# Kernel tuning notes

Measured on AMD Instinct MI355X. Metric: run time of the kernel, lower is better.

Reference implementation:

```python
import jax, jax.numpy as jnp
import numpy as np

DIM, HEADS, HD = 256, 8, 32
WS, GT, SR = 8, 1, 2
B_, H0, W0 = 4, 128, 128
SCALE = HD ** -0.5


def _bilinear_up_align(x, s):
    # x: (B, C, h, w) -> (B, C, h*s, w*s), bilinear, align_corners=True (matches torch)
    B, C, h, w = x.shape
    oh, ow = h * s, w * s
    def coords(n, o):
        pos = jnp.arange(o, dtype=jnp.float32) * ((n - 1) / (o - 1))
        i0 = jnp.clip(jnp.floor(pos).astype(jnp.int32), 0, n - 2)
        t = pos - i0.astype(jnp.float32)
        return i0, t
    y0, ty = coords(h, oh)
    x0, tx = coords(w, ow)
    top = x[:, :, y0, :] * (1 - ty)[:, None] + x[:, :, y0 + 1, :] * ty[:, None]
    return top[:, :, :, x0] * (1 - tx) + top[:, :, :, x0 + 1] * tx


def _layernorm(x, w, b, eps=1e-5):
    mu = x.mean(-1, keepdims=True)
    var = x.var(-1, keepdims=True)
    return (x - mu) * jax.lax.rsqrt(var + eps) * w + b


def setup_inputs() -> dict:
    key = jax.random.key(0)
    ks = jax.random.split(key, 8)
    w = lambda k, shape: jax.random.normal(k, shape, jnp.float32) * 0.02
    return {
        "x": jax.random.normal(ks[0], (B_, H0 * W0, DIM), jnp.float32),
        "gt": jax.random.normal(ks[1], (B_, H0 // WS, W0 // WS, GT, DIM), jnp.float32),
        "q_w": w(ks[2], (DIM, DIM)), "q_b": jnp.zeros((DIM,), jnp.float32),
        "kv_w": w(ks[3], (2 * DIM, DIM)), "kv_b": jnp.zeros((2 * DIM,), jnp.float32),
        "sr_w": w(ks[4], (DIM, DIM, SR, SR)), "sr_b": jnp.zeros((DIM,), jnp.float32),
        "norm_w": jnp.ones((DIM,), jnp.float32), "norm_b": jnp.zeros((DIM,), jnp.float32),
        "proj_w": w(ks[5], (DIM, DIM)), "proj_b": jnp.zeros((DIM,), jnp.float32),
        "H": H0, "W": W0,
    }


def reference(x, gt, q_w, q_b, kv_w, kv_b, sr_w, sr_b, norm_w, norm_b, proj_w, proj_b, H, W):
    Bb, Np, C = x.shape
    nH, nW = H // WS, W // WS  # H, W multiples of WS -> no padding branch
    xm = x.reshape(Bb, H, W, C)
    # window partition -> (B, WS*WS, C), B = Bb*nH*nW
    xw = xm.reshape(Bb, nH, WS, nW, WS, C).transpose(0, 1, 3, 2, 4, 5).reshape(-1, WS * WS, C)
    g = gt.reshape(-1, GT, C)  # gt grid already matches (nH, nW)
    skip = g
    xc = jnp.concatenate([g, xw], axis=1)  # (B, N, C), N = GT + WS*WS
    B, N, _ = xc.shape
    q = (xc @ q_w.T + q_b).reshape(B, N, HEADS, HD).transpose(0, 2, 1, 3)  # (B,h,N,d)
    # spatial-reduction KV branch (sr_ratio > 1, gt_num != 0)
    x_ = xw.transpose(0, 2, 1).reshape(B, C, WS, WS)
    x_ = _bilinear_up_align(x_, SR)  # (B, C, WS*SR, WS*SR)
    x_ = jax.lax.conv_general_dilated(
        x_, sr_w, (SR, SR), "VALID",
        dimension_numbers=("NCHW", "OIHW", "NCHW")) + sr_b[None, :, None, None]  # (B,C,WS,WS)
    x_ = _layernorm(x_.reshape(B, C, -1).transpose(0, 2, 1), norm_w, norm_b)
    x_ = jnp.concatenate([g, x_], axis=1)  # (B, N, C)
    kv = (x_ @ kv_w.T + kv_b).reshape(B, -1, 2, HEADS, HD).transpose(2, 0, 3, 1, 4)
    k, v = kv[0], kv[1]  # (B,h,N,d)
    attn = jax.nn.softmax(jnp.einsum("bhnd,bhmd->bhnm", q, k) * SCALE, axis=-1)
    out = jnp.einsum("bhnm,bhmd->bhnd", attn, v).transpose(0, 2, 1, 3).reshape(B, N, C)
    out = out @ proj_w.T + proj_b
    gt_out = out[:, :GT, :]
    xo = out[:, GT:, :].reshape(Bb, nH, nW, WS, WS, C)
    xo = xo.transpose(0, 1, 3, 2, 4, 5).reshape(Bb, H, W, C)  # window reverse
    return xo.reshape(Bb, H * W, C), gt_out, skip
```

## Files before the change

### kernel.cpp

```cpp
#include <hip/hip_runtime.h>

typedef __attribute__((ext_vector_type(4))) float f32x4;
typedef __attribute__((ext_vector_type(8))) short bf16x8;
typedef __attribute__((ext_vector_type(2))) uint u32x2;

#define SCALE_ 0.17677669529663687f

__device__ __forceinline__ float bf2f(ushort u){
  union { unsigned i; float f; } v; v.i = ((unsigned)u) << 16; return v.f;
}
__device__ __forceinline__ ushort f2bf(float f){
  union { float f; unsigned i; } v; v.f = f;
  unsigned r = v.i + 0x7fffu + ((v.i >> 16) & 1u);
  return (ushort)(r >> 16);
}
__device__ __forceinline__ void gl16(const void* g, const ushort* l) {
  __builtin_amdgcn_global_load_lds((const __attribute__((address_space(1))) uint*)g,
                                   (__attribute__((address_space(3))) uint*)l, 16, 0, 0);
}

__global__ __launch_bounds__(256) void k_prep(const float* __restrict__ x,
    const float* __restrict__ gt, ushort* __restrict__ xc,
    ushort* __restrict__ xkv, float* __restrict__ out2)
{
  int row = blockIdx.x;
  int c = threadIdx.x;
  int wi = row / 65, n = row - wi * 65;
  if (n == 0) {
    float g = gt[(size_t)wi * 256 + c];
    ushort gb = f2bf(g);
    xc[(size_t)row * 256 + c] = gb;
    xkv[(size_t)row * 256 + c] = gb;
    out2[(size_t)wi * 256 + c] = g;
  } else {
    int s = n - 1, r = s >> 3, cc = s & 7;
    int b = wi >> 8, wh = (wi >> 4) & 15, ww = wi & 15;
    int hw = (wh * 8 + r) * 128 + ww * 8 + cc;
    xc[(size_t)row * 256 + c] = f2bf(x[((size_t)b * 16384 + hw) * 256 + c]);
  }
}

__global__ __launch_bounds__(256) void k_wprep(const float* __restrict__ qw,
    const float* __restrict__ kvw, const float* __restrict__ pw,
    const float* __restrict__ srw, ushort* __restrict__ wq,
    ushort* __restrict__ wkv, ushort* __restrict__ wpr, ushort* __restrict__ wcv)
{
  int i = blockIdx.x * 256 + threadIdx.x;
  if (i < 65536)            wq[i] = f2bf(qw[i]);
  else if (i < 196608)      wkv[i - 65536] = f2bf(kvw[i - 65536]);
  else if (i < 262144)      wpr[i - 196608] = f2bf(pw[i - 196608]);
  else {
    int j = i - 262144;
    int o = j >> 10, t = (j >> 8) & 3, cc = j & 255;
    wcv[j] = f2bf(srw[o * 1024 + cc * 4 + t]);
  }
}

template<int N>
__global__ __launch_bounds__(256) void k_gemm2(const ushort* __restrict__ A,
    const ushort* __restrict__ W, const float* __restrict__ bias,
    ushort* __restrict__ C)
{
  constexpr int K = 256;
  __shared__ __align__(16) ushort As[2][128 * 64];
  __shared__ __align__(16) ushort Bs[2][128 * 64];
  int lin = blockIdx.y * gridDim.x + blockIdx.x;
  int qq = (gridDim.x * gridDim.y) >> 3;
  int sw2 = (lin & 7) * qq + (lin >> 3);
  int m0 = (sw2 / gridDim.x) * 128, n0 = (sw2 % gridDim.x) * 128;
  int tid = threadIdx.x, lane = tid & 63;
  int wave = tid >> 6;
  int lm = lane & 15, kg = lane >> 4;
  int wr = wave >> 1, wc = wave & 1;

  const char* Ab = (const char*)A + (size_t)m0 * (K * 2);
  const char* Bb = (const char*)W + (size_t)n0 * (K * 2);

  auto stage = [&](int buf, int kt) {
#pragma unroll
    for (int j = 0; j < 4; ++j) {
      int c = j * 256 + tid;
      int row = c >> 3, slot = c & 7;
      int srcoff = row * (K * 2) + kt * 128 + ((slot * 16) ^ ((row & 7) << 4));
      gl16(Ab + srcoff, (const ushort*)((const char*)As[buf] + c * 16));
      gl16(Bb + srcoff, (const ushort*)((const char*)Bs[buf] + c * 16));
    }
  };

  f32x4 acc[4][4];
  f32x4 zero = {0.f, 0.f, 0.f, 0.f};
#pragma unroll
  for (int a = 0; a < 4; ++a)
#pragma unroll
    for (int b = 0; b < 4; ++b) acc[a][b] = zero;

  stage(0, 0);
  __syncthreads();
#pragma unroll
  for (int t = 0; t < 4; ++t) {
    int cur = t & 1;
    if (t < 3) stage(cur ^ 1, t + 1);
#pragma unroll
    for (int s = 0; s < 2; ++s) {
      int sw = (lm & 7) << 4;
      bf16x8 af[4], bw[4];
#pragma unroll
      for (int mi = 0; mi < 4; ++mi) {
        int row = wr * 64 + mi * 16 + lm;
        af[mi] = *(const bf16x8*)((const char*)As[cur] + row * 128 + ((s * 64 + kg * 16) ^ sw));
      }
#pragma unroll
      for (int ni = 0; ni < 4; ++ni) {
        int row = wc * 64 + ni * 16 + lm;
        bw[ni] = *(const bf16x8*)((const char*)Bs[cur] + row * 128 + ((s * 64 + kg * 16) ^ sw));
      }
#pragma unroll
      for (int mi = 0; mi < 4; ++mi)
#pragma unroll
        for (int ni = 0; ni < 4; ++ni)
          acc[mi][ni] = __builtin_amdgcn_mfma_f32_16x16x32_bf16(af[mi], bw[ni], acc[mi][ni], 0, 0, 0);
    }
    __syncthreads();
  }

  int rbase = m0 + wr * 64 + kg * 4;
#pragma unroll
  for (int ni = 0; ni < 4; ++ni) {
    int col = n0 + wc * 64 + ni * 16 + lm;
    float bv = bias[col];
#pragma unroll
    for (int mi = 0; mi < 4; ++mi) {
#pragma unroll
      for (int r = 0; r < 4; ++r)
        C[(size_t)(rbase + mi * 16 + r) * N + col] = f2bf(acc[mi][ni][r] + bv);
    }
  }
}

__global__ __launch_bounds__(512) void k_conv(const ushort* __restrict__ xc,
    const ushort* __restrict__ wconv, ushort* __restrict__ cconv)
{
  __shared__ ushort U[2][64 * 256];
  int wi = blockIdx.x;
  int tid = threadIdx.x, wave = tid >> 6, lane = tid & 63;
  int lm = lane & 15, kg = lane >> 4;
  const ushort* src = xc + (size_t)(wi * 65 + 1) * 256;
  f32x4 acc[4][2];
  f32x4 zero = {0.f, 0.f, 0.f, 0.f};
#pragma unroll
  for (int a = 0; a < 4; a++)
#pragma unroll
    for (int b = 0; b < 2; b++) acc[a][b] = zero;

  int cb = (tid & 31) * 8;
  int sg = tid >> 5;

  auto build = [&](int t, ushort* Ub) {
    int dy = t >> 1, dx = t & 1;
    for (int s = sg; s < 64; s += 16) {
      int i = s >> 3, j = s & 7;
      int yy = 2 * i + dy, xx = 2 * j + dx;
      float py = yy * (7.0f / 15.0f); int iy = (int)py; if (iy > 6) iy = 6; float ty = py - iy;
      float px = xx * (7.0f / 15.0f); int ix = (int)px; if (ix > 6) ix = 6; float tx = px - ix;
      float w00 = (1.f - ty) * (1.f - tx), w01 = (1.f - ty) * tx;
      float w10 = ty * (1.f - tx), w11 = ty * tx;
      const ushort* p = src + (size_t)(iy * 8 + ix) * 256 + cb;
      bf16x8 p00 = *(const bf16x8*)(p);
      bf16x8 p01 = *(const bf16x8*)(p + 256);
      bf16x8 p10 = *(const bf16x8*)(p + 2048);
      bf16x8 p11 = *(const bf16x8*)(p + 2304);
      bf16x8 o8;
#pragma unroll
      for (int jj = 0; jj < 8; jj++) {
        float v = w00 * bf2f((ushort)p00[jj]) + w01 * bf2f((ushort)p01[jj])
                + w10 * bf2f((ushort)p10[jj]) + w11 * bf2f((ushort)p11[jj]);
        o8[jj] = (short)f2bf(v);
      }
      int byteoff = s * 512 + ((2 * cb) ^ ((s & 7) << 4));
      *(bf16x8*)((char*)Ub + byteoff) = o8;
    }
  };

  build(0, U[0]);
  __syncthreads();
  for (int t = 0; t < 4; t++) {
    const ushort* Ub = U[t & 1];
    const ushort* wc = wconv + t * 256;
    for (int kk = 0; kk < 256; kk += 32) {
      int kb = kk + kg * 8;
      bf16x8 afr[4];
#pragma unroll
      for (int mi = 0; mi < 4; mi++) {
        int srow = mi * 16 + lm;
        int off = (srow * 512 + 2 * kb) ^ ((srow & 7) << 4);
        afr[mi] = *(const bf16x8*)((const char*)Ub + off);
      }
#pragma unroll
      for (int ni = 0; ni < 2; ni++) {
        bf16x8 b = *(const bf16x8*)(wc + (size_t)(wave * 32 + ni * 16 + lm) * 1024 + kb);
#pragma unroll
        for (int mi = 0; mi < 4; mi++)
          acc[mi][ni] = __builtin_amdgcn_mfma_f32_16x16x32_bf16(afr[mi], b, acc[mi][ni], 0, 0, 0);
      }
    }
    if (t < 3) build(t + 1, U[(t + 1) & 1]);
    __syncthreads();
  }

#pragma unroll
  for (int mi = 0; mi < 4; mi++) {
    int row = wi * 64 + mi * 16 + kg * 4;
#pragma unroll
    for (int ni = 0; ni < 2; ni++) {
      int col = wave * 32 + ni * 16 + lm;
#pragma unroll
      for (int r = 0; r < 4; r++)
        cconv[(size_t)(row + r) * 256 + col] = f2bf(acc[mi][ni][r]);
    }
  }
}

__global__ __launch_bounds__(256) void k_ln(const ushort* __restrict__ cconv,
    const float* __restrict__ srb, const float* __restrict__ nw,
    const float* __restrict__ nb, ushort* __restrict__ xkv)
{
  int row = blockIdx.x * 4 + (threadIdx.x >> 6);
  int lane = threadIdx.x & 63;
  const ushort* p = cconv + (size_t)row * 256;
  float v[4]; float sum = 0.f, sq = 0.f;
#pragma unroll
  for (int r = 0; r < 4; r++) {
    int c = r * 64 + lane;
    v[r] = bf2f(p[c]) + srb[c];
    sum += v[r]; sq += v[r] * v[r];
  }
#pragma unroll
  for (int off = 1; off < 64; off <<= 1) {
    sum += __shfl_xor(sum, off, 64);
    sq  += __shfl_xor(sq,  off, 64);
  }
  float mean = sum * (1.f / 256.f);
  float var = sq * (1.f / 256.f) - mean * mean;
  float rs = rsqrtf(var + 1e-5f);
  int wi = row >> 6, s = row & 63;
  ushort* o = xkv + (size_t)(wi * 65 + 1 + s) * 256;
#pragma unroll
  for (int r = 0; r < 4; r++) {
    int c = r * 64 + lane;
    o[c] = f2bf((v[r] - mean) * rs * nw[c] + nb[c]);
  }
}

__global__ __launch_bounds__(256) void k_attn(const ushort* __restrict__ q,
    const ushort* __restrict__ kv, ushort* __restrict__ att)
{
  __shared__ ushort smem[4][8064];
  int wi = blockIdx.x >> 1;
  int tid = threadIdx.x, wave = tid >> 6, lane = tid & 63;
  int h = (blockIdx.x & 1) * 4 + wave;
  int lm = lane & 15, kg = lane >> 4;
  ushort* plds = smem[wave];
  ushort* vt   = smem[wave] + 5760;

  size_t qbase  = (size_t)wi * 65 * 256 + (size_t)h * 32;
  size_t kvbase = (size_t)wi * 65 * 512 + (size_t)h * 32;

  for (int e = lane; e < 2080; e += 64) {
    int m = e >> 5, d = e & 31;
    vt[d * 72 + m] = kv[kvbase + (size_t)m * 512 + 256 + d];
  }

  bf16x8 akf[5], bqf[5];
#pragma unroll
  for (int i = 0; i < 5; i++) {
    akf[i] = *(const bf16x8*)(kv + kvbase + (size_t)(16 * i + lm) * 512 + kg * 8);
    bqf[i] = *(const bf16x8*)(q  + qbase  + (size_t)(16 * i + lm) * 256 + kg * 8);
  }

  f32x4 sc[5][5];
  f32x4 zero = {0.f, 0.f, 0.f, 0.f};
#pragma unroll
  for (int mi = 0; mi < 5; mi++)
#pragma unroll
    for (int nj = 0; nj < 5; nj++) sc[mi][nj] = zero;
#pragma unroll
  for (int mi = 0; mi < 5; mi++)
#pragma unroll
    for (int nj = 0; nj < 5; nj++)
      sc[mi][nj] = __builtin_amdgcn_mfma_f32_16x16x32_bf16(akf[mi], bqf[nj], sc[mi][nj], 0, 0, 0);

  const float C = SCALE_ * 1.4426950408889634f;
  float inv[5], p64b[5];
#pragma unroll
  for (int nj = 0; nj < 5; nj++) {
    float s4 = sc[4][nj][0];
    float mx = (kg == 0) ? s4 : -1e30f;
#pragma unroll
    for (int mi = 0; mi < 4; mi++)
#pragma unroll
      for (int r = 0; r < 4; r++) mx = fmaxf(mx, sc[mi][nj][r]);
    mx = fmaxf(mx, __shfl_xor(mx, 16, 64));
    mx = fmaxf(mx, __shfl_xor(mx, 32, 64));
    float sum = 0.f;
#pragma unroll
    for (int mi = 0; mi < 4; mi++)
#pragma unroll
      for (int r = 0; r < 4; r++) {
        float e = exp2f((sc[mi][nj][r] - mx) * C);
        sc[mi][nj][r] = e; sum += e;
      }
    float e4 = exp2f((s4 - mx) * C);
    sum += (kg == 0) ? e4 : 0.f;
    sum += __shfl_xor(sum, 16, 64);
    sum += __shfl_xor(sum, 32, 64);
    inv[nj] = 1.0f / sum;
    p64b[nj] = __shfl(e4, lm, 64);
  }

#pragma unroll
  for (int nj = 0; nj < 5; nj++) {
    int n = 16 * nj + lm;
#pragma unroll
    for (int mi = 0; mi < 4; mi++) {
      uint lo = (uint)f2bf(sc[mi][nj][0]) | ((uint)f2bf(sc[mi][nj][1]) << 16);
      uint hi = (uint)f2bf(sc[mi][nj][2]) | ((uint)f2bf(sc[mi][nj][3]) << 16);
      u32x2 pk = {lo, hi};
      *(u32x2*)(plds + n * 72 + 16 * mi + 4 * kg) = pk;
    }
  }

  f32x4 od[2][5];
#pragma unroll
  for (int dt = 0; dt < 2; dt++)
#pragma unroll
    for (int nj = 0; nj < 5; nj++) od[dt][nj] = zero;
#pragma unroll
  for (int c = 0; c < 2; c++) {
    bf16x8 av[2], bp[5];
#pragma unroll
    for (int dt = 0; dt < 2; dt++)
      av[dt] = *(const bf16x8*)(vt + (16 * dt + lm) * 72 + c * 32 + kg * 8);
#pragma unroll
    for (int nj = 0; nj < 5; nj++)
      bp[nj] = *(const bf16x8*)(plds + (16 * nj + lm) * 72 + c * 32 + kg * 8);
#pragma unroll
    for (int dt = 0; dt < 2; dt++)
#pragma unroll
      for (int nj = 0; nj < 5; nj++)
        od[dt][nj] = __builtin_amdgcn_mfma_f32_16x16x32_bf16(av[dt], bp[nj], od[dt][nj], 0, 0, 0);
  }
  float v64[8];
#pragma unroll
  for (int dt = 0; dt < 2; dt++)
#pragma unroll
    for (int r = 0; r < 4; r++)
      v64[dt * 4 + r] = bf2f(vt[(16 * dt + 4 * kg + r) * 72 + 64]);
#pragma unroll
  for (int dt = 0; dt < 2; dt++)
#pragma unroll
    for (int nj = 0; nj < 5; nj++)
#pragma unroll
      for (int r = 0; r < 4; r++)
        od[dt][nj][r] += v64[dt * 4 + r] * p64b[nj];

#pragma unroll
  for (int nj = 0; nj < 5; nj++) {
    int n = 16 * nj + lm;
    float scl = inv[nj];
#pragma unroll
    for (int dt = 0; dt < 2; dt++) {
      uint lo = (uint)f2bf(od[dt][nj][0] * scl) | ((uint)f2bf(od[dt][nj][1] * scl) << 16);
      uint hi = (uint)f2bf(od[dt][nj][2] * scl) | ((uint)f2bf(od[dt][nj][3] * scl) << 16);
      u32x2 pk = {lo, hi};
      *(u32x2*)(plds + n * 40 + 16 * dt + 4 * kg) = pk;
    }
  }
  size_t abase = (size_t)wi * 65 * 256 + (size_t)h * 32;
  for (int e = lane; e < 1040; e += 64) {
    int n = e >> 4, d2 = e & 15;
    *(uint*)(att + abase + (size_t)n * 256 + 2 * d2) = *(const uint*)(plds + n * 40 + 2 * d2);
  }
}

__global__ __launch_bounds__(256) void k_scatter(const ushort* __restrict__ po,
    float* __restrict__ out)
{
  size_t e = (size_t)blockIdx.x * 256 + threadIdx.x;
  if (e < 16777216) {
    int c = (int)(e & 255);
    int hw = (int)((e >> 8) & 16383);
    int b = (int)(e >> 22);
    int hh = hw >> 7, wp = hw & 127;
    int wh = hh >> 3, r = hh & 7, ww = wp >> 3, cc = wp & 7;
    int wi = b * 256 + wh * 16 + ww;
    int n = 1 + r * 8 + cc;
    out[e] = bf2f(po[(size_t)(wi * 65 + n) * 256 + c]);
  } else {
    size_t e2 = e - 16777216;
    int wi = (int)(e2 >> 8), c = (int)(e2 & 255);
    out[e] = bf2f(po[(size_t)(wi * 65) * 256 + c]);
  }
}

extern "C" void kernel_launch(void* const* d_in, const int* in_sizes, int n_in,
                              void* d_out, int out_size, void* d_ws, size_t ws_size,
                              hipStream_t stream)
{
  const float* x    = (const float*)d_in[0];
  const float* gt   = (const float*)d_in[1];
  const float* q_w  = (const float*)d_in[2];
  const float* q_b  = (const float*)d_in[3];
  const float* kv_w = (const float*)d_in[4];
  const float* kv_b = (const float*)d_in[5];
  const float* sr_w = (const float*)d_in[6];
  const float* sr_b = (const float*)d_in[7];
  const float* nw   = (const float*)d_in[8];
  const float* nb   = (const float*)d_in[9];
  const float* p_w  = (const float*)d_in[10];
  const float* p_b  = (const float*)d_in[11];
  (void)in_sizes; (void)n_in; (void)out_size;

  if (ws_size < 204996608u) return;
  char* ws = (char*)d_ws;
  ushort* xc  = (ushort*)(ws);
  ushort* qb  = (ushort*)(ws + 34078720);
  ushort* xkv = (ushort*)(ws + 68157440);
  ushort* kv  = (ushort*)(ws + 102236160);
  ushort* ccv = (ushort*)(ws + 170393600);
  ushort* wq  = (ushort*)(ws + 203948032);
  ushort* wkv = (ushort*)(ws + 204079104);
  ushort* wpr = (ushort*)(ws + 204341248);
  ushort* wcv = (ushort*)(ws + 204472320);

  float* out = (float*)d_out;
  float* out2 = out + 16777216 + 262144;

  k_prep<<<66560, 256, 0, stream>>>(x, gt, xc, xkv, out2);
  k_wprep<<<2048, 256, 0, stream>>>(q_w, kv_w, p_w, sr_w, wq, wkv, wpr, wcv);
  k_gemm2<256><<<dim3(2, 520), 256, 0, stream>>>(xc, wq, q_b, qb);
  k_conv<<<1024, 512, 0, stream>>>(xc, wcv, ccv);
  k_ln<<<16384, 256, 0, stream>>>(ccv, sr_b, nw, nb, xkv);
  k_gemm2<512><<<dim3(4, 520), 256, 0, stream>>>(xkv, wkv, kv_b, kv);
  k_attn<<<2048, 256, 0, stream>>>(qb, kv, xc);
  k_gemm2<256><<<dim3(2, 520), 256, 0, stream>>>(xc, wpr, p_b, qb);
  k_scatter<<<66560, 256, 0, stream>>>(qb, out);
}
```

Before: 280.0 us.

## Separable bilinear upsample in conv kernel, build two taps per pass

The conv kernel's LDS builder now does the bilinear upsample separably. Each thread interpolates vertically once over a row strip of five source pixels, then produces eight horizontal outputs from those values. This cuts redundant global loads and multiplies compared with four-corner gathers per output. Each build now fills both dx phases for a given dy into the two LDS buffers, so the loop becomes two build/MFMA phases with an extra barrier and no build overlapped with MFMA. A launch-bounds occupancy hint of 4 is added, which may constrain registers given the larger per-thread H array.

```diff
diff --git a/kernel.cpp b/kernel.cpp
--- a/kernel.cpp
+++ b/kernel.cpp
@@ -137,14 +137,15 @@
   }
 }
 
-__global__ __launch_bounds__(512) void k_conv(const ushort* __restrict__ xc,
+__global__ __launch_bounds__(512, 4) void k_conv(const ushort* __restrict__ xc,
     const ushort* __restrict__ wconv, ushort* __restrict__ cconv)
 {
-  __shared__ ushort U[2][64 * 256];
+  __shared__ __align__(16) ushort U[2][64 * 256];
   int wi = blockIdx.x;
   int tid = threadIdx.x, wave = tid >> 6, lane = tid & 63;
   int lm = lane & 15, kg = lane >> 4;
   const ushort* src = xc + (size_t)(wi * 65 + 1) * 256;
+
   f32x4 acc[4][2];
   f32x4 zero = {0.f, 0.f, 0.f, 0.f};
 #pragma unroll
@@ -152,60 +153,77 @@
 #pragma unroll
     for (int b = 0; b < 2; b++) acc[a][b] = zero;
 
-  int cb = (tid & 31) * 8;
-  int sg = tid >> 5;
-
-  auto build = [&](int t, ushort* Ub) {
-    int dy = t >> 1, dx = t & 1;
-    for (int s = sg; s < 64; s += 16) {
-      int i = s >> 3, j = s & 7;
-      int yy = 2 * i + dy, xx = 2 * j + dx;
-      float py = yy * (7.0f / 15.0f); int iy = (int)py; if (iy > 6) iy = 6; float ty = py - iy;
+  int cg = lane & 31;
+  int half = lane >> 5;
+  int xh = wave & 1;
+  int yy2 = (wave >> 1) * 2 + half;
+
+  auto build = [&](int p) {
+    int yy = yy2 * 2 + p;
+    float py = yy * (7.0f / 15.0f); int iy = (int)py; if (iy > 6) iy = 6; float ty = py - iy;
+    int j0 = xh * 3;
+    const ushort* r0 = src + (size_t)(iy * 8 + j0) * 256 + cg * 8;
+    const ushort* r1 = r0 + 2048;
+    float H[5][8];
+#pragma unroll
+    for (int jj = 0; jj < 5; ++jj) {
+      bf16x8 a = *(const bf16x8*)(r0 + jj * 256);
+      bf16x8 b = *(const bf16x8*)(r1 + jj * 256);
+#pragma unroll
+      for (int e = 0; e < 8; ++e) {
+        float av = bf2f((ushort)a[e]);
+        H[jj][e] = av + ty * (bf2f((ushort)b[e]) - av);
+      }
+    }
+#pragma unroll
+    for (int xi = 0; xi < 8; ++xi) {
+      int xx = xh * 8 + xi;
       float px = xx * (7.0f / 15.0f); int ix = (int)px; if (ix > 6) ix = 6; float tx = px - ix;
-      float w00 = (1.f - ty) * (1.f - tx), w01 = (1.f - ty) * tx;
-      float w10 = ty * (1.f - tx), w11 = ty * tx;
-      const ushort* p = src + (size_t)(iy * 8 + ix) * 256 + cb;
-      bf16x8 p00 = *(const bf16x8*)(p);
-      bf16x8 p01 = *(const bf16x8*)(p + 256);
-      bf16x8 p10 = *(const bf16x8*)(p + 2048);
-      bf16x8 p11 = *(const bf16x8*)(p + 2304);
+      int hl = ix - j0;
       bf16x8 o8;
 #pragma unroll
-      for (int jj = 0; jj < 8; jj++) {
-        float v = w00 * bf2f((ushort)p00[jj]) + w01 * bf2f((ushort)p01[jj])
-                + w10 * bf2f((ushort)p10[jj]) + w11 * bf2f((ushort)p11[jj]);
-        o8[jj] = (short)f2bf(v);
-      }
-      int byteoff = s * 512 + ((2 * cb) ^ ((s & 7) << 4));
-      *(bf16x8*)((char*)Ub + byteoff) = o8;
+      for (int e = 0; e < 8; ++e) {
+        float lv = H[hl][e];
+        o8[e] = (short)f2bf(lv + tx * (H[hl + 1][e] - lv));
+      }
+      int s = yy2 * 8 + (xx >> 1);
+      int off = (xx & 1) * 32768 + s * 512 + ((cg * 16) ^ ((s & 7) << 4));
+      *(bf16x8*)((char*)U + off) = o8;
     }
   };
 
-  build(0, U[0]);
+  auto mfma_pair = [&](int p) {
+#pragma unroll
+    for (int tt = 0; tt < 2; ++tt) {
+      const ushort* Ub = U[tt];
+      const ushort* wc = wconv + (p * 2 + tt) * 256;
+      for (int kk = 0; kk < 256; kk += 32) {
+        int kb = kk + kg * 8;
+        bf16x8 afr[4];
+#pragma unroll
+        for (int mi = 0; mi < 4; mi++) {
+          int srow = mi * 16 + lm;
+          int off = (srow * 512 + 2 * kb) ^ ((srow & 7) << 4);
+          afr[mi] = *(const bf16x8*)((const char*)Ub + off);
+        }
+#pragma unroll
+        for (int ni = 0; ni < 2; ni++) {
+          bf16x8 b = *(const bf16x8*)(wc + (size_t)(wave * 32 + ni * 16 + lm) * 1024 + kb);
+#pragma unroll
+          for (int mi = 0; mi < 4; mi++)
+            acc[mi][ni] = __builtin_amdgcn_mfma_f32_16x16x32_bf16(afr[mi], b, acc[mi][ni], 0, 0, 0);
+        }
+      }
+    }
+  };
+
+  build(0);
   __syncthreads();
-  for (int t = 0; t < 4; t++) {
-    const ushort* Ub = U[t & 1];
-    const ushort* wc = wconv + t * 256;
-    for (int kk = 0; kk < 256; kk += 32) {
-      int kb = kk + kg * 8;
-      bf16x8 afr[4];
-#pragma unroll
-      for (int mi = 0; mi < 4; mi++) {
-        int srow = mi * 16 + lm;
-        int off = (srow * 512 + 2 * kb) ^ ((srow & 7) << 4);
-        afr[mi] = *(const bf16x8*)((const char*)Ub + off);
-      }
-#pragma unroll
-      for (int ni = 0; ni < 2; ni++) {
-        bf16x8 b = *(const bf16x8*)(wc + (size_t)(wave * 32 + ni * 16 + lm) * 1024 + kb);
-#pragma unroll
-        for (int mi = 0; mi < 4; mi++)
-          acc[mi][ni] = __builtin_amdgcn_mfma_f32_16x16x32_bf16(afr[mi], b, acc[mi][ni], 0, 0, 0);
-      }
-    }
-    if (t < 3) build(t + 1, U[(t + 1) & 1]);
-    __syncthreads();
-  }
+  mfma_pair(0);
+  __syncthreads();
+  build(1);
+  __syncthreads();
+  mfma_pair(1);
 
 #pragma unroll
   for (int mi = 0; mi < 4; mi++) {
```

Result: slower. 345.2 us (+23.3%).

## Stage conv source window in LDS and use separable bilinear interpolation

Applied to the files above, without the earlier changes.

The conv kernel now copies the 64x256 bf16 window into LDS with async global_load_lds, then builds each upsampled tap from LDS. It does the bilinear interpolation separably, with a vertical lerp per row that is reused across columns and horizontal weights fixed at compile time, instead of four global gathers per output. The double-buffered U tile becomes a single buffer, so build and MFMA no longer overlap and extra barriers are added. It also forces waves_per_eu(4,4).

```diff
diff --git a/kernel.cpp b/kernel.cpp
--- a/kernel.cpp
+++ b/kernel.cpp
@@ -1,6 +1,7 @@
 #include <hip/hip_runtime.h>
 
 typedef __attribute__((ext_vector_type(4))) float f32x4;
+typedef __attribute__((ext_vector_type(8))) float f32x8;
 typedef __attribute__((ext_vector_type(8))) short bf16x8;
 typedef __attribute__((ext_vector_type(2))) uint u32x2;
 
@@ -137,14 +138,89 @@
   }
 }
 
-__global__ __launch_bounds__(512) void k_conv(const ushort* __restrict__ xc,
+__device__ __forceinline__ f32x8 row_lerp(const char* srcS, int row, int cg, float ty) {
+  int a0 = row * 512 + ((cg * 16) ^ ((row & 7) << 4));
+  int a1 = (row + 8) * 512 + ((cg * 16) ^ ((row & 7) << 4));
+  bf16x8 a = *(const bf16x8*)(srcS + a0);
+  bf16x8 b = *(const bf16x8*)(srcS + a1);
+  f32x8 h;
+#pragma unroll
+  for (int e = 0; e < 8; ++e) {
+    float av = bf2f((ushort)a[e]);
+    h[e] = av + ty * (bf2f((ushort)b[e]) - av);
+  }
+  return h;
+}
+__device__ __forceinline__ void emit_u(char* U, const f32x8& Ha, const f32x8& Hb,
+                                       float tx, int s, int cg) {
+  bf16x8 o8;
+#pragma unroll
+  for (int e = 0; e < 8; ++e) {
+    float lv = Ha[e];
+    o8[e] = (short)f2bf(lv + tx * (Hb[e] - lv));
+  }
+  *(bf16x8*)(U + s * 512 + ((cg * 16) ^ ((s & 7) << 4))) = o8;
+}
+
+template<int XH, int DX>
+__device__ __forceinline__ void conv_build(const char* srcS, char* U,
+                                           int dy, int i, int cg)
+{
+  int yy = 2 * i + dy;
+  float py = yy * (7.0f / 15.0f);
+  int iy = (int)py; if (iy > 6) iy = 6;
+  float ty = py - iy;
+  constexpr int j0 = XH * 3;
+  int rb = iy * 8 + j0;
+  f32x8 H0 = row_lerp(srcS, rb + 0, cg, ty);
+  f32x8 H1 = row_lerp(srcS, rb + 1, cg, ty);
+  f32x8 H2 = row_lerp(srcS, rb + 2, cg, ty);
+  f32x8 H3 = row_lerp(srcS, rb + 3, cg, ty);
+  f32x8 H4 = row_lerp(srcS, rb + 4, cg, ty);
+  int sb = i * 8 + XH * 4;
+  if (XH == 0 && DX == 0) {
+    emit_u(U, H0, H1, 0.0f,        sb + 0, cg);
+    emit_u(U, H0, H1, 14.f / 15.f, sb + 1, cg);
+    emit_u(U, H1, H2, 13.f / 15.f, sb + 2, cg);
+    emit_u(U, H2, H3, 12.f / 15.f, sb + 3, cg);
+  } else if (XH == 0 && DX == 1) {
+    emit_u(U, H0, H1,  7.f / 15.f, sb + 0, cg);
+    emit_u(U, H1, H2,  6.f / 15.f, sb + 1, cg);
+    emit_u(U, H2, H3,  5.f / 15.f, sb + 2, cg);
+    emit_u(U, H3, H4,  4.f / 15.f, sb + 3, cg);
+  } else if (XH == 1 && DX == 0) {
+    emit_u(U, H0, H1, 11.f / 15.f, sb + 0, cg);
+    emit_u(U, H1, H2, 10.f / 15.f, sb + 1, cg);
+    emit_u(U, H2, H3,  9.f / 15.f, sb + 2, cg);
+    emit_u(U, H3, H4,  8.f / 15.f, sb + 3, cg);
+  } else {
+    emit_u(U, H1, H2,  3.f / 15.f, sb + 0, cg);
+    emit_u(U, H2, H3,  2.f / 15.f, sb + 1, cg);
+    emit_u(U, H3, H4,  1.f / 15.f, sb + 2, cg);
+    emit_u(U, H3, H4,  1.0f,       sb + 3, cg);
+  }
+}
+
+__global__ __launch_bounds__(512)
+__attribute__((amdgpu_waves_per_eu(4, 4)))
+void k_conv(const ushort* __restrict__ xc,
     const ushort* __restrict__ wconv, ushort* __restrict__ cconv)
 {
-  __shared__ ushort U[2][64 * 256];
+  __shared__ __align__(16) ushort srcS[64 * 256];
+  __shared__ __align__(16) ushort Ubuf[64 * 256];
   int wi = blockIdx.x;
   int tid = threadIdx.x, wave = tid >> 6, lane = tid & 63;
   int lm = lane & 15, kg = lane >> 4;
-  const ushort* src = xc + (size_t)(wi * 65 + 1) * 256;
+
+  const char* src_g = (const char*)(xc + (size_t)(wi * 65 + 1) * 256);
+#pragma unroll
+  for (int j = 0; j < 4; ++j) {
+    int c = j * 512 + tid;
+    int row = c >> 5, slot = c & 31;
+    int srcoff = row * 512 + ((slot * 16) ^ ((row & 7) << 4));
+    gl16(src_g + srcoff, (const ushort*)((const char*)srcS + c * 16));
+  }
+
   f32x4 acc[4][2];
   f32x4 zero = {0.f, 0.f, 0.f, 0.f};
 #pragma unroll
@@ -152,39 +228,11 @@
 #pragma unroll
     for (int b = 0; b < 2; b++) acc[a][b] = zero;
 
-  int cb = (tid & 31) * 8;
-  int sg = tid >> 5;
-
-  auto build = [&](int t, ushort* Ub) {
-    int dy = t >> 1, dx = t & 1;
-    for (int s = sg; s < 64; s += 16) {
-      int i = s >> 3, j = s & 7;
-      int yy = 2 * i + dy, xx = 2 * j + dx;
-      float py = yy * (7.0f / 15.0f); int iy = (int)py; if (iy > 6) iy = 6; float ty = py - iy;
-      float px = xx * (7.0f / 15.0f); int ix = (int)px; if (ix > 6) ix = 6; float tx = px - ix;
-      float w00 = (1.f - ty) * (1.f - tx), w01 = (1.f - ty) * tx;
-      float w10 = ty * (1.f - tx), w11 = ty * tx;
-      const ushort* p = src + (size_t)(iy * 8 + ix) * 256 + cb;
-      bf16x8 p00 = *(const bf16x8*)(p);
-      bf16x8 p01 = *(const bf16x8*)(p + 256);
-      bf16x8 p10 = *(const bf16x8*)(p + 2048);
-      bf16x8 p11 = *(const bf16x8*)(p + 2304);
-      bf16x8 o8;
-#pragma unroll
-      for (int jj = 0; jj < 8; jj++) {
-        float v = w00 * bf2f((ushort)p00[jj]) + w01 * bf2f((ushort)p01[jj])
-                + w10 * bf2f((ushort)p10[jj]) + w11 * bf2f((ushort)p11[jj]);
-        o8[jj] = (short)f2bf(v);
-      }
-      int byteoff = s * 512 + ((2 * cb) ^ ((s & 7) << 4));
-      *(bf16x8*)((char*)Ub + byteoff) = o8;
-    }
-  };
-
-  build(0, U[0]);
-  __syncthreads();
-  for (int t = 0; t < 4; t++) {
-    const ushort* Ub = U[t & 1];
+  int cg = tid & 31;
+  int i = (tid >> 5) & 7;
+  int xh = tid >> 8;
+
+  auto mfma_tap = [&](int t) {
     const ushort* wc = wconv + t * 256;
     for (int kk = 0; kk < 256; kk += 32) {
       int kb = kk + kg * 8;
@@ -193,7 +241,7 @@
       for (int mi = 0; mi < 4; mi++) {
         int srow = mi * 16 + lm;
         int off = (srow * 512 + 2 * kb) ^ ((srow & 7) << 4);
-        afr[mi] = *(const bf16x8*)((const char*)Ub + off);
+        afr[mi] = *(const bf16x8*)((const char*)Ubuf + off);
       }
 #pragma unroll
       for (int ni = 0; ni < 2; ni++) {
@@ -203,9 +251,29 @@
           acc[mi][ni] = __builtin_amdgcn_mfma_f32_16x16x32_bf16(afr[mi], b, acc[mi][ni], 0, 0, 0);
       }
     }
-    if (t < 3) build(t + 1, U[(t + 1) & 1]);
-    __syncthreads();
-  }
+  };
+
+  __syncthreads();
+
+  if (xh == 0) conv_build<0, 0>((const char*)srcS, (char*)Ubuf, 0, i, cg);
+  else         conv_build<1, 0>((const char*)srcS, (char*)Ubuf, 0, i, cg);
+  __syncthreads();
+  mfma_tap(0);
+  __syncthreads();
+  if (xh == 0) conv_build<0, 1>((const char*)srcS, (char*)Ubuf, 0, i, cg);
+  else         conv_build<1, 1>((const char*)srcS, (char*)Ubuf, 0, i, cg);
+  __syncthreads();
+  mfma_tap(1);
+  __syncthreads();
+  if (xh == 0) conv_build<0, 0>((const char*)srcS, (char*)Ubuf, 1, i, cg);
+  else         conv_build<1, 0>((const char*)srcS, (char*)Ubuf, 1, i, cg);
+  __syncthreads();
+  mfma_tap(2);
+  __syncthreads();
+  if (xh == 0) conv_build<0, 1>((const char*)srcS, (char*)Ubuf, 1, i, cg);
+  else         conv_build<1, 1>((const char*)srcS, (char*)Ubuf, 1, i, cg);
+  __syncthreads();
+  mfma_tap(3);
 
 #pragma unroll
   for (int mi = 0; mi < 4; mi++) {
```

Result: faster. 274.0 us (-2.2%).

## Fuse output projection with window-reverse scatter and merge weight prep into input prep

Applied to the files above, without the earlier changes.

The final projection GEMM now writes fp32 results straight to their window-reversed positions in the output, removing the bf16 intermediate and the separate scatter kernel. Weight conversion is folded into the input-prep kernel as extra blocks, and input prep is vectorised to float4 reads with four rows per block. This cuts one full read/write pass over a large activation tensor and two launches. The fused epilogue's stores are strided per row, so they may coalesce less well than the old scatter.

```diff
diff --git a/kernel.cpp b/kernel.cpp
--- a/kernel.cpp
+++ b/kernel.cpp
@@ -1,6 +1,7 @@
 #include <hip/hip_runtime.h>
 
 typedef __attribute__((ext_vector_type(4))) float f32x4;
+typedef __attribute__((ext_vector_type(8))) float f32x8;
 typedef __attribute__((ext_vector_type(8))) short bf16x8;
 typedef __attribute__((ext_vector_type(2))) uint u32x2;
 
@@ -20,39 +21,47 @@
 }
 
 __global__ __launch_bounds__(256) void k_prep(const float* __restrict__ x,
-    const float* __restrict__ gt, ushort* __restrict__ xc,
-    ushort* __restrict__ xkv, float* __restrict__ out2)
-{
-  int row = blockIdx.x;
-  int c = threadIdx.x;
+    const float* __restrict__ gt, const float* __restrict__ qw,
+    const float* __restrict__ kvw, const float* __restrict__ pw,
+    const float* __restrict__ srw, ushort* __restrict__ xc,
+    ushort* __restrict__ xkv, float* __restrict__ out2,
+    ushort* __restrict__ wq, ushort* __restrict__ wkv,
+    ushort* __restrict__ wpr, ushort* __restrict__ wcv)
+{
+  int blk = blockIdx.x;
+  int tid = threadIdx.x;
+  if (blk >= 16640) {
+    int i = (blk - 16640) * 256 + tid;
+    if (i < 65536)            wq[i] = f2bf(qw[i]);
+    else if (i < 196608)      wkv[i - 65536] = f2bf(kvw[i - 65536]);
+    else if (i < 262144)      wpr[i - 196608] = f2bf(pw[i - 196608]);
+    else {
+      int j = i - 262144;
+      int o = j >> 10, t = (j >> 8) & 3, cc = j & 255;
+      wcv[j] = f2bf(srw[o * 1024 + cc * 4 + t]);
+    }
+    return;
+  }
+  int row = blk * 4 + (tid >> 6);
+  int c4 = (tid & 63) * 4;
   int wi = row / 65, n = row - wi * 65;
   if (n == 0) {
-    float g = gt[(size_t)wi * 256 + c];
-    ushort gb = f2bf(g);
-    xc[(size_t)row * 256 + c] = gb;
-    xkv[(size_t)row * 256 + c] = gb;
-    out2[(size_t)wi * 256 + c] = g;
+    float4 g4 = *(const float4*)(gt + (size_t)wi * 256 + c4);
+    uint lo = (uint)f2bf(g4.x) | ((uint)f2bf(g4.y) << 16);
+    uint hi = (uint)f2bf(g4.z) | ((uint)f2bf(g4.w) << 16);
+    u32x2 pk = {lo, hi};
+    *(u32x2*)(xc  + (size_t)row * 256 + c4) = pk;
+    *(u32x2*)(xkv + (size_t)row * 256 + c4) = pk;
+    *(float4*)(out2 + (size_t)wi * 256 + c4) = g4;
   } else {
     int s = n - 1, r = s >> 3, cc = s & 7;
     int b = wi >> 8, wh = (wi >> 4) & 15, ww = wi & 15;
     int hw = (wh * 8 + r) * 128 + ww * 8 + cc;
-    xc[(size_t)row * 256 + c] = f2bf(x[((size_t)b * 16384 + hw) * 256 + c]);
-  }
-}
-
-__global__ __launch_bounds__(256) void k_wprep(const float* __restrict__ qw,
-    const float* __restrict__ kvw, const float* __restrict__ pw,
-    const float* __restrict__ srw, ushort* __restrict__ wq,
-    ushort* __restrict__ wkv, ushort* __restrict__ wpr, ushort* __restrict__ wcv)
-{
-  int i = blockIdx.x * 256 + threadIdx.x;
-  if (i < 65536)            wq[i] = f2bf(qw[i]);
-  else if (i < 196608)      wkv[i - 65536] = f2bf(kvw[i - 65536]);
-  else if (i < 262144)      wpr[i - 196608] = f2bf(pw[i - 196608]);
-  else {
-    int j = i - 262144;
-    int o = j >> 10, t = (j >> 8) & 3, cc = j & 255;
-    wcv[j] = f2bf(srw[o * 1024 + cc * 4 + t]);
+    float4 v4 = *(const float4*)(x + ((size_t)b * 16384 + hw) * 256 + c4);
+    uint lo = (uint)f2bf(v4.x) | ((uint)f2bf(v4.y) << 16);
+    uint hi = (uint)f2bf(v4.z) | ((uint)f2bf(v4.w) << 16);
+    u32x2 pk = {lo, hi};
+    *(u32x2*)(xc + (size_t)row * 256 + c4) = pk;
   }
 }
 
@@ -133,6 +142,99 @@
 #pragma unroll
       for (int r = 0; r < 4; ++r)
         C[(size_t)(rbase + mi * 16 + r) * N + col] = f2bf(acc[mi][ni][r] + bv);
+    }
+  }
+}
+
+__global__ __launch_bounds__(256) void k_gemm_out(const ushort* __restrict__ A,
+    const ushort* __restrict__ W, const float* __restrict__ bias,
+    float* __restrict__ out)
+{
+  constexpr int K = 256;
+  __shared__ __align__(16) ushort As[2][128 * 64];
+  __shared__ __align__(16) ushort Bs[2][128 * 64];
+  int lin = blockIdx.y * gridDim.x + blockIdx.x;
+  int qq = (gridDim.x * gridDim.y) >> 3;
+  int sw2 = (lin & 7) * qq + (lin >> 3);
+  int m0 = (sw2 / gridDim.x) * 128, n0 = (sw2 % gridDim.x) * 128;
+  int tid = threadIdx.x, lane = tid & 63;
+  int wave = tid >> 6;
+  int lm = lane & 15, kg = lane >> 4;
+  int wr = wave >> 1, wc = wave & 1;
+
+  const char* Ab = (const char*)A + (size_t)m0 * (K * 2);
+  const char* Bb = (const char*)W + (size_t)n0 * (K * 2);
+
+  auto stage = [&](int buf, int kt) {
+#pragma unroll
+    for (int j = 0; j < 4; ++j) {
+      int c = j * 256 + tid;
+      int row = c >> 3, slot = c & 7;
+      int srcoff = row * (K * 2) + kt * 128 + ((slot * 16) ^ ((row & 7) << 4));
+      gl16(Ab + srcoff, (const ushort*)((const char*)As[buf] + c * 16));
+      gl16(Bb + srcoff, (const ushort*)((const char*)Bs[buf] + c * 16));
+    }
+  };
+
+  f32x4 acc[4][4];
+  f32x4 zero = {0.f, 0.f, 0.f, 0.f};
+#pragma unroll
+  for (int a = 0; a < 4; ++a)
+#pragma unroll
+    for (int b = 0; b < 4; ++b) acc[a][b] = zero;
+
+  stage(0, 0);
+  __syncthreads();
+#pragma unroll
+  for (int t = 0; t < 4; ++t) {
+    int cur = t & 1;
+    if (t < 3) stage(cur ^ 1, t + 1);
+#pragma unroll
+    for (int s = 0; s < 2; ++s) {
+      int sw = (lm & 7) << 4;
+      bf16x8 af[4], bw[4];
+#pragma unroll
+      for (int mi = 0; mi < 4; ++mi) {
+        int row = wr * 64 + mi * 16 + lm;
+        af[mi] = *(const bf16x8*)((const char*)As[cur] + row * 128 + ((s * 64 + kg * 16) ^ sw));
+      }
+#pragma unroll
+      for (int ni = 0; ni < 4; ++ni) {
+        int row = wc * 64 + ni * 16 + lm;
+        bw[ni] = *(const bf16x8*)((const char*)Bs[cur] + row * 128 + ((s * 64 + kg * 16) ^ sw));
+      }
+#pragma unroll
+      for (int mi = 0; mi < 4; ++mi)
+#pragma unroll
+        for (int ni = 0; ni < 4; ++ni)
+          acc[mi][ni] = __builtin_amdgcn_mfma_f32_16x16x32_bf16(af[mi], bw[ni], acc[mi][ni], 0, 0, 0);
+    }
+    __syncthreads();
+  }
+
+  int rbase = m0 + wr * 64 + kg * 4;
+#pragma unroll
+  for (int mi = 0; mi < 4; ++mi) {
+#pragma unroll
+    for (int r = 0; r < 4; ++r) {
+      int g = rbase + mi * 16 + r;
+      int wi2 = g / 65;
+      int n = g - wi2 * 65;
+      size_t dstrow;
+      if (n == 0) {
+        dstrow = (size_t)(16777216 >> 8) + wi2;
+      } else {
+        int s = n - 1;
+        int b = wi2 >> 8, wh = (wi2 >> 4) & 15, ww = wi2 & 15;
+        int r2 = s >> 3, cc = s & 7;
+        dstrow = (size_t)(b << 14) + (wh * 8 + r2) * 128 + ww * 8 + cc;
+      }
+      float* dst = out + dstrow * 256;
+#pragma unroll
+      for (int ni = 0; ni < 4; ++ni) {
+        int col = n0 + wc * 64 + ni * 16 + lm;
+        dst[col] = acc[mi][ni][r] + bias[col];
+      }
     }
   }
 }
@@ -382,26 +484,6 @@
   }
 }
 
-__global__ __launch_bounds__(256) void k_scatter(const ushort* __restrict__ po,
-    float* __restrict__ out)
-{
-  size_t e = (size_t)blockIdx.x * 256 + threadIdx.x;
-  if (e < 16777216) {
-    int c = (int)(e & 255);
-    int hw = (int)((e >> 8) & 16383);
-    int b = (int)(e >> 22);
-    int hh = hw >> 7, wp = hw & 127;
-    int wh = hh >> 3, r = hh & 7, ww = wp >> 3, cc = wp & 7;
-    int wi = b * 256 + wh * 16 + ww;
-    int n = 1 + r * 8 + cc;
-    out[e] = bf2f(po[(size_t)(wi * 65 + n) * 256 + c]);
-  } else {
-    size_t e2 = e - 16777216;
-    int wi = (int)(e2 >> 8), c = (int)(e2 & 255);
-    out[e] = bf2f(po[(size_t)(wi * 65) * 256 + c]);
-  }
-}
-
 extern "C" void kernel_launch(void* const* d_in, const int* in_sizes, int n_in,
                               void* d_out, int out_size, void* d_ws, size_t ws_size,
                               hipStream_t stream)
@@ -435,13 +517,12 @@
   float* out = (float*)d_out;
   float* out2 = out + 16777216 + 262144;
 
-  k_prep<<<66560, 256, 0, stream>>>(x, gt, xc, xkv, out2);
-  k_wprep<<<2048, 256, 0, stream>>>(q_w, kv_w, p_w, sr_w, wq, wkv, wpr, wcv);
+  k_prep<<<18688, 256, 0, stream>>>(x, gt, q_w, kv_w, p_w, sr_w,
+                                    xc, xkv, out2, wq, wkv, wpr, wcv);
   k_gemm2<256><<<dim3(2, 520), 256, 0, stream>>>(xc, wq, q_b, qb);
   k_conv<<<1024, 512, 0, stream>>>(xc, wcv, ccv);
   k_ln<<<16384, 256, 0, stream>>>(ccv, sr_b, nw, nb, xkv);
   k_gemm2<512><<<dim3(4, 520), 256, 0, stream>>>(xkv, wkv, kv_b, kv);
   k_attn<<<2048, 256, 0, stream>>>(qb, kv, xc);
-  k_gemm2<256><<<dim3(2, 520), 256, 0, stream>>>(xc, wpr, p_b, qb);
-  k_scatter<<<66560, 256, 0, stream>>>(qb, out);
-}
+  k_gemm_out<<<dim3(2, 520), 256, 0, stream>>>(xc, wpr, p_b, out);
+}
```

New measurement: 240.2 us. 14.2% less time.
